# Optimization experiments

Measured on AMD Instinct MI355X. Metric: run time of the kernel, lower is better.

Reference implementation:

```python
import jax, jax.numpy as jnp
import numpy as np

NEG_SLOPE = 0.2  # PyG GATv2Conv default


def with_self_loops(edge_index, n):
    loop = jnp.arange(n, dtype=edge_index.dtype)
    src = jnp.concatenate([edge_index[0], loop])
    dst = jnp.concatenate([edge_index[1], loop])
    return src, dst


def gatv2(x, src, dst, Wl, bl, Wr, br, att, bias):
    """PyG GATv2Conv (eval mode, concat=True, add_self_loops done by caller).
    x: [N, F_in]; att: [H, C]. Returns [N, H*C]."""
    N = x.shape[0]
    H, C = att.shape
    xl = (x @ Wl + bl).reshape(N, H, C)  # lin_l(x): source-side transform
    xr = (x @ Wr + br).reshape(N, H, C)  # lin_r(x): target-side transform
    s = jax.nn.leaky_relu(xl[src] + xr[dst], NEG_SLOPE)      # [E,H,C]
    logit = jnp.einsum('ehc,hc->eh', s, att)                 # [E,H]
    m = jax.ops.segment_max(logit, dst, num_segments=N)      # stable softmax per target
    e = jnp.exp(logit - m[dst])
    den = jax.ops.segment_sum(e, dst, num_segments=N)
    alpha = e / (den[dst] + 1e-16)                           # [E,H]
    out = jax.ops.segment_sum(alpha[:, :, None] * xl[src], dst, num_segments=N)
    return out.reshape(N, H * C) + bias


def setup_inputs() -> dict:
    N, E = 20000, 320000        # agent nodes / edges
    M, EM = 40000, 400000       # lane nodes / edges
    B, L = 64, 50               # focal agents, centerline length
    SEQ, INC, HID, HEADS, OUT = 50, 2, 32, 4, 60
    H4 = HID * HEADS
    key = jax.random.key(0)
    ks = list(jax.random.split(key, 48))
    kit = iter(ks)

    def p(shape):
        return jax.random.normal(next(kit), shape, jnp.float32) * 0.05

    inp = {
        'x': jax.random.normal(next(kit), (N, SEQ, INC), jnp.float32),
        'edge_index': jax.random.randint(next(kit), (2, E), 0, N),
        'lane_x': jax.random.normal(next(kit), (M, 2), jnp.float32),
        'lane_edge_index': jax.random.randint(next(kit), (2, EM), 0, M),
        'batch': jnp.sort(jax.random.randint(next(kit), (N,), 0, B)),
        'focal_idx': jax.random.randint(next(kit), (B,), 0, N),
        'centerlines': jax.random.normal(next(kit), (B, L, 2), jnp.float32),
        # agent embedding
        'ae_W': p((SEQ * INC, HID)), 'ae_b': p((HID,)),
        # agent subgraph conv1 / conv2
        'a1_Wl': p((HID, H4)), 'a1_bl': p((H4,)), 'a1_Wr': p((HID, H4)), 'a1_br': p((H4,)), 'a1_att': p((HEADS, HID)), 'a1_b': p((H4,)),
        'a2_Wl': p((H4, H4)), 'a2_bl': p((H4,)), 'a2_Wr': p((H4, H4)), 'a2_br': p((H4,)), 'a2_att': p((HEADS, HID)), 'a2_b': p((H4,)),
        # map embedding + map subgraph
        'me_W': p((2, HID)), 'me_b': p((HID,)),
        'm1_Wl': p((HID, H4)), 'm1_bl': p((H4,)), 'm1_Wr': p((HID, H4)), 'm1_br': p((H4,)), 'm1_att': p((HEADS, HID)), 'm1_b': p((H4,)),
        'm2_Wl': p((H4, H4)), 'm2_bl': p((H4,)), 'm2_Wr': p((H4, H4)), 'm2_br': p((H4,)), 'm2_att': p((HEADS, HID)), 'm2_b': p((H4,)),
        # centerline processor
        'cl_W': p((2, HID)), 'cl_b': p((HID,)),
        # global graph (heads=1)
        'g_Wl': p((H4, HID)), 'g_bl': p((HID,)), 'g_Wr': p((H4, HID)), 'g_br': p((HID,)), 'g_att': p((1, HID)), 'g_b': p((HID,)),
        # output head
        'fc_W': p((2 * HID, OUT)), 'fc_b': p((OUT,)),
    }
    return inp


def reference(x, edge_index, lane_x, lane_edge_index, batch, focal_idx, centerlines,
              ae_W, ae_b,
              a1_Wl, a1_bl, a1_Wr, a1_br, a1_att, a1_b,
              a2_Wl, a2_bl, a2_Wr, a2_br, a2_att, a2_b,
              me_W, me_b,
              m1_Wl, m1_bl, m1_Wr, m1_br, m1_att, m1_b,
              m2_Wl, m2_bl, m2_Wr, m2_br, m2_att, m2_b,
              cl_W, cl_b,
              g_Wl, g_bl, g_Wr, g_br, g_att, g_b,
              fc_W, fc_b):
    N = x.shape[0]
    M = lane_x.shape[0]
    # agent branch
    agent_x = jax.nn.relu(x.reshape(N, -1) @ ae_W + ae_b)
    a_src, a_dst = with_self_loops(edge_index, N)
    h = jax.nn.relu(gatv2(agent_x, a_src, a_dst, a1_Wl, a1_bl, a1_Wr, a1_br, a1_att, a1_b))
    agent_features = jax.nn.relu(gatv2(h, a_src, a_dst, a2_Wl, a2_bl, a2_Wr, a2_br, a2_att, a2_b))  # [N,128]
    # map branch (output unused downstream in original, computed for faithfulness)
    map_x = jax.nn.relu(lane_x @ me_W + me_b)
    m_src, m_dst = with_self_loops(lane_edge_index, M)
    hm = jax.nn.relu(gatv2(map_x, m_src, m_dst, m1_Wl, m1_bl, m1_Wr, m1_br, m1_att, m1_b))
    map_features = jax.nn.relu(gatv2(hm, m_src, m_dst, m2_Wl, m2_bl, m2_Wr, m2_br, m2_att, m2_b))
    _ = map_features  # global_mean_pool results are dead code in the original forward
    # global graph over agent features (heads=1)
    global_features = jax.nn.relu(gatv2(agent_features, a_src, a_dst, g_Wl, g_bl, g_Wr, g_br, g_att, g_b))  # [N,32]
    focal = global_features[focal_idx]  # [B,32]
    # centerlines: per-polyline mean then linear (no relu, as in original)
    cl_feat = jnp.mean(centerlines, axis=1) @ cl_W + cl_b  # [B,32]
    combined = jnp.concatenate([focal, cl_feat], axis=1)
    return combined @ fc_W + fc_b
```

## Files before the change

### kernel.cpp

```cpp
#include <hip/hip_runtime.h>
#include <hip/hip_bf16.h>
#include <hip/hip_fp16.h>
#include <math.h>

typedef __hip_bfloat16 bf16;
#define NEG_SLOPE 0.2f
#define SFLAG (1 << 30)

typedef _Float16 f16x8 __attribute__((ext_vector_type(8)));
typedef float f32x4 __attribute__((ext_vector_type(4)));

__global__ void k_detect_zero(const unsigned short* __restrict__ x, int* __restrict__ flag,
                              int* __restrict__ zbase, int n) {
    for (int i = blockIdx.x * blockDim.x + threadIdx.x; i < n; i += gridDim.x * blockDim.x)
        zbase[i] = 0;
    if (blockIdx.x == 0) {
        __shared__ int cnt;
        if (threadIdx.x == 0) cnt = 0;
        __syncthreads();
        int local = 0;
        for (int i = threadIdx.x; i < 2048; i += blockDim.x) {
            unsigned short w = x[2 * i];
            int e = (w >> 7) & 0xFF;
            if (e >= 0x90) local++;
        }
        atomicAdd(&cnt, local);
        __syncthreads();
        if (threadIdx.x == 0) flag[0] = (cnt > 100) ? 1 : 0;
    }
}

#define NSEG 25
struct Seg { const void* src; int n; int off; };
struct Tab { Seg s[NSEG]; };

__device__ __forceinline__ float ldconv(const void* src, int i, int f32mode) {
    return f32mode ? ((const float*)src)[i]
                   : __bfloat162float(((const bf16*)src)[i]);
}

__global__ void k_convert(Tab tab, float* __restrict__ dst, const int* __restrict__ flag,
                          const int* __restrict__ dstArr, int E, int N,
                          int* __restrict__ deg, int* __restrict__ rank,
                          const void* a2WlS, const void* a2WrS,
                          const void* gWlS, const void* gWrS,
                          __half* __restrict__ a2Wlt, __half* __restrict__ a2Wrt,
                          __half* __restrict__ gWlt, __half* __restrict__ gWrt) {
    int f32mode = flag[0];
    int gid = blockIdx.x * blockDim.x + threadIdx.x;
    int gsz = gridDim.x * blockDim.x;
    for (int s = 0; s < NSEG; s++) {
        Seg sg = tab.s[s];
        for (int i = gid; i < sg.n; i += gsz) {
            dst[sg.off + i] = ldconv(sg.src, i, f32mode);
        }
    }
    for (int i = gid; i < 128 * 128; i += gsz) {
        int k = i >> 7, j = i & 127;
        a2Wlt[(size_t)j * 128 + k] = __float2half(ldconv(a2WlS, i, f32mode));
        a2Wrt[(size_t)j * 128 + k] = __float2half(ldconv(a2WrS, i, f32mode));
    }
    for (int i = gid; i < 128 * 32; i += gsz) {
        int k = i >> 5, j = i & 31;
        gWlt[(size_t)j * 128 + k] = __float2half(ldconv(gWlS, i, f32mode));
        gWrt[(size_t)j * 128 + k] = __float2half(ldconv(gWrS, i, f32mode));
    }
    int EA = E + N;
    for (int e = gid; e < EA; e += gsz) {
        int d = (e < E) ? dstArr[e] : (e - E);
        rank[e] = atomicAdd(&deg[d], 1);
    }
}

__launch_bounds__(1024)
__global__ void k_scanf(const int* __restrict__ deg, int* __restrict__ offs,
                        int n, int* __restrict__ st, int nb) {
    __shared__ int ws[16];
    __shared__ int stot, sprev;
    int tile = blockIdx.x;
    int i = tile * 1024 + threadIdx.x;
    int lane = threadIdx.x & 63, wid = threadIdx.x >> 6;
    int v = (i < n) ? deg[i] : 0;
    int x = v;
    #pragma unroll
    for (int o = 1; o < 64; o <<= 1) {
        int y = __shfl_up(x, o);
        if (lane >= o) x += y;
    }
    if (lane == 63) ws[wid] = x;
    __syncthreads();
    if (wid == 0) {
        int w = (lane < 16) ? ws[lane] : 0;
        int s = w;
        #pragma unroll
        for (int o = 1; o < 16; o <<= 1) {
            int y = __shfl_up(s, o);
            if (lane >= o) s += y;
        }
        if (lane < 16) ws[lane] = s - w;
        if (lane == 15) stot = s;
    }
    __syncthreads();
    int local = ws[wid] + x - v;
    if (threadIdx.x == 0) {
        int prev = 0;
        if (tile > 0) {
            int vv;
            while ((((vv = __hip_atomic_load(&st[tile - 1], __ATOMIC_ACQUIRE,
                                             __HIP_MEMORY_SCOPE_AGENT))) & SFLAG) == 0) {}
            prev = vv & ~SFLAG;
        }
        __hip_atomic_store(&st[tile], (prev + stot) | SFLAG, __ATOMIC_RELEASE,
                           __HIP_MEMORY_SCOPE_AGENT);
        sprev = prev;
        if (tile == nb - 1) offs[n] = prev + stot;
    }
    __syncthreads();
    if (i < n) offs[i] = sprev + local;
}

__launch_bounds__(256)
__global__ void k_fill_embedlin(const int* __restrict__ srcArr, const int* __restrict__ dstArr,
                                int E, int N, const int* __restrict__ offs,
                                const int* __restrict__ rank, int* __restrict__ csr,
                                const void* __restrict__ xraw, const int* __restrict__ flag,
                                const float* __restrict__ aeW, const float* __restrict__ aeb,
                                const float* __restrict__ Wl, const float* __restrict__ bl,
                                const float* __restrict__ Wr, const float* __restrict__ br,
                                __half* __restrict__ outl, float* __restrict__ outr,
                                int EB) {
    __shared__ float xs[100 * 36];
    __shared__ float axs[32 * 36];
    if (blockIdx.x >= EB) {
        int e = (blockIdx.x - EB) * 256 + threadIdx.x;
        int EA = E + N;
        if (e >= EA) return;
        int d, s;
        if (e < E) { d = dstArr[e]; s = srcArr[e]; } else { d = s = e - E; }
        csr[offs[d] + rank[e]] = s;
        return;
    }
    constexpr int NTP = 36;
    int t = threadIdx.x, nb = blockIdx.x * 32;
    if (flag[0]) {
        const float4* x4 = (const float4*)xraw;
        for (int idx = t; idx < 32 * 25; idx += 256) {
            int node = idx / 25, k4 = idx % 25;
            float4 v = x4[(size_t)(nb + node) * 25 + k4];
            xs[(k4 * 4 + 0) * NTP + node] = v.x;
            xs[(k4 * 4 + 1) * NTP + node] = v.y;
            xs[(k4 * 4 + 2) * NTP + node] = v.z;
            xs[(k4 * 4 + 3) * NTP + node] = v.w;
        }
    } else {
        const ushort4* xu = (const ushort4*)xraw;
        for (int idx = t; idx < 32 * 25; idx += 256) {
            int node = idx / 25, k4 = idx % 25;
            ushort4 u = xu[(size_t)(nb + node) * 25 + k4];
            xs[(k4 * 4 + 0) * NTP + node] = __uint_as_float((unsigned)u.x << 16);
            xs[(k4 * 4 + 1) * NTP + node] = __uint_as_float((unsigned)u.y << 16);
            xs[(k4 * 4 + 2) * NTP + node] = __uint_as_float((unsigned)u.z << 16);
            xs[(k4 * 4 + 3) * NTP + node] = __uint_as_float((unsigned)u.w << 16);
        }
    }
    __syncthreads();
    {
        int j = t & 31, g0 = t >> 5;
        float a0 = 0.f, a1 = 0.f, a2 = 0.f, a3 = 0.f;
        #pragma unroll 10
        for (int k = 0; k < 100; k++) {
            float w = aeW[k * 32 + j];
            const float4 xv = *(const float4*)&xs[k * NTP + g0 * 4];
            a0 += w * xv.x; a1 += w * xv.y; a2 += w * xv.z; a3 += w * xv.w;
        }
        float bj = aeb[j];
        axs[j * NTP + g0 * 4 + 0] = fmaxf(a0 + bj, 0.f);
        axs[j * NTP + g0 * 4 + 1] = fmaxf(a1 + bj, 0.f);
        axs[j * NTP + g0 * 4 + 2] = fmaxf(a2 + bj, 0.f);
        axs[j * NTP + g0 * 4 + 3] = fmaxf(a3 + bj, 0.f);
    }
    __syncthreads();
    {
        int j = t & 63, g0 = t >> 6;
        float aL0[2][4], aL1[2][4], aR0[2][4], aR1[2][4];
        #pragma unroll
        for (int g = 0; g < 2; g++)
            #pragma unroll
            for (int c = 0; c < 4; c++) { aL0[g][c]=0.f; aL1[g][c]=0.f; aR0[g][c]=0.f; aR1[g][c]=0.f; }
        #pragma unroll 4
        for (int k = 0; k < 32; k++) {
            float wl0 = Wl[k * 128 + j];
            float wl1 = Wl[k * 128 + j + 64];
            float wr0 = Wr[k * 128 + j];
            float wr1 = Wr[k * 128 + j + 64];
            #pragma unroll
            for (int g = 0; g < 2; g++) {
                const float4 xv = *(const float4*)&axs[k * NTP + (g0 + g * 4) * 4];
                aL0[g][0] += wl0 * xv.x; aL0[g][1] += wl0 * xv.y; aL0[g][2] += wl0 * xv.z; aL0[g][3] += wl0 * xv.w;
                aL1[g][0] += wl1 * xv.x; aL1[g][1] += wl1 * xv.y; aL1[g][2] += wl1 * xv.z; aL1[g][3] += wl1 * xv.w;
                aR0[g][0] += wr0 * xv.x; aR0[g][1] += wr0 * xv.y; aR0[g][2] += wr0 * xv.z; aR0[g][3] += wr0 * xv.w;
                aR1[g][0] += wr1 * xv.x; aR1[g][1] += wr1 * xv.y; aR1[g][2] += wr1 * xv.z; aR1[g][3] += wr1 * xv.w;
            }
        }
        float bl0 = bl[j], bl1 = bl[j + 64], br0 = br[j], br1 = br[j + 64];
        #pragma unroll
        for (int g = 0; g < 2; g++) {
            int n0 = nb + (g0 + g * 4) * 4;
            #pragma unroll
            for (int c = 0; c < 4; c++) {
                size_t row = (size_t)(n0 + c) * 128;
                outl[row + j]      = __float2half(aL0[g][c] + bl0);
                outl[row + j + 64] = __float2half(aL1[g][c] + bl1);
                outr[row + j]      = aR0[g][c] + br0;
                outr[row + j + 64] = aR1[g][c] + br1;
            }
        }
    }
}

__device__ __forceinline__ void gat_proc(float4 raw, bool valid,
                                         const float* xrd, const float* av,
                                         float* acc, float& sm) {
    const __half2* h = (const __half2*)&raw;
    float v[8];
    float2 f;
    f = __half22float2(h[0]); v[0] = f.x; v[1] = f.y;
    f = __half22float2(h[1]); v[2] = f.x; v[3] = f.y;
    f = __half22float2(h[2]); v[4] = f.x; v[5] = f.y;
    f = __half22float2(h[3]); v[6] = f.x; v[7] = f.y;
    float p = 0.f;
    #pragma unroll
    for (int c = 0; c < 8; c++) {
        float u = v[c] + xrd[c];
        u = (u > 0.f) ? u : NEG_SLOPE * u;
        p += u * av[c];
    }
    p += __shfl_xor(p, 1);
    p += __shfl_xor(p, 2);
    p += __shfl_xor(p, 4);
    p += __shfl_xor(p, 8);
    float w = __expf(fminf(p, 80.f));
    if (!valid) w = 0.f;
    sm += w;
    #pragma unroll
    for (int c = 0; c < 8; c++) acc[c] += w * v[c];
}

__device__ __forceinline__ void gat16_to_lds(__half* xsh,
                                             const __half* __restrict__ xl,
                                             const float* __restrict__ xr,
                                             const float* __restrict__ att,
                                             const int* __restrict__ offs,
                                             const int* __restrict__ csr,
                                             const float* __restrict__ bias,
                                             int d, int node) {
    int t = threadIdx.x;
    int lane = t & 63;
    int sub = lane & 15;
    int lb = lane & 48;
    float av[8];
    {
        const float4* t4 = (const float4*)(att + sub * 8);
        float4 c = t4[0], e = t4[1];
        av[0]=c.x; av[1]=c.y; av[2]=c.z; av[3]=c.w;
        av[4]=e.x; av[5]=e.y; av[6]=e.z; av[7]=e.w;
    }
    bool ok = d >= 0;
    int i0 = ok ? offs[d] : 0;
    int i1 = ok ? offs[d + 1] : 0;
    int cnt = i1 - i0;

    float xrd[8];
    #pragma unroll
    for (int c = 0; c < 8; c++) xrd[c] = 0.f;
    if (ok) {
        const float4* p4 = (const float4*)(xr + (size_t)d * 128 + sub * 8);
        float4 a = p4[0], b = p4[1];
        xrd[0]=a.x; xrd[1]=a.y; xrd[2]=a.z; xrd[3]=a.w;
        xrd[4]=b.x; xrd[5]=b.y; xrd[6]=b.z; xrd[7]=b.w;
    }
    float acc[8];
    #pragma unroll
    for (int c = 0; c < 8; c++) acc[c] = 0.f;
    float sm = 0.f;

    int myv = (sub < cnt) ? csr[i0 + sub] : 0;
    for (int c0 = 0; c0 < cnt; c0 += 16) {
        int myv_nxt = (c0 + 16 + sub < cnt) ? csr[i0 + c0 + 16 + sub] : 0;
        int rem = min(cnt - c0, 16);
        for (int k = 0; k < rem; k += 4) {
            int s0 = __shfl(myv, lb + k + 0);
            int s1 = __shfl(myv, lb + k + 1);
            int s2 = __shfl(myv, lb + k + 2);
            int s3 = __shfl(myv, lb + k + 3);
            float4 r0 = *(const float4*)(xl + (size_t)s0 * 128 + sub * 8);
            float4 r1 = *(const float4*)(xl + (size_t)s1 * 128 + sub * 8);
            float4 r2 = *(const float4*)(xl + (size_t)s2 * 128 + sub * 8);
            float4 r3 = *(const float4*)(xl + (size_t)s3 * 128 + sub * 8);
            gat_proc(r0, true,        xrd, av, acc, sm);
            gat_proc(r1, k + 1 < rem, xrd, av, acc, sm);
            gat_proc(r2, k + 2 < rem, xrd, av, acc, sm);
            gat_proc(r3, k + 3 < rem, xrd, av, acc, sm);
        }
        myv = myv_nxt;
    }

    int ch = sub * 8;
    if (ok) {
        float inv = 1.f / (sm + 1e-16f);
        #pragma unroll
        for (int c = 0; c < 8; c += 2) {
            __half2 hv;
            hv.x = __float2half(fmaxf(acc[c]     * inv + bias[ch + c],     0.f));
            hv.y = __float2half(fmaxf(acc[c + 1] * inv + bias[ch + c + 1], 0.f));
            *(__half2*)&xsh[node * 136 + ch + c] = hv;
        }
    } else {
        #pragma unroll
        for (int c = 0; c < 8; c += 2)
            *(__half2*)&xsh[node * 136 + ch + c] = __half2{__half(0.f), __half(0.f)};
    }
}

__launch_bounds__(256)
__global__ void k_gatlin(const __half* __restrict__ xl, const float* __restrict__ xr,
                         const float* __restrict__ att,
                         const int* __restrict__ offs, const int* __restrict__ csr,
                         const float* __restrict__ bias,
                         const __half* __restrict__ Wlt, const float* __restrict__ bl,
                         const __half* __restrict__ Wrt, const float* __restrict__ br,
                         __half* __restrict__ outl, float* __restrict__ outr, int N,
                         const int* __restrict__ focal, int B,
                         int* __restrict__ L, int* __restrict__ Lcnt, int GT) {
    if (blockIdx.x >= GT) {
        int t = threadIdx.x;
        if (t < B) {
            int f = focal[t];
            int j0 = offs[f], j1 = offs[f + 1];
            int base = atomicAdd(Lcnt, j1 - j0);
            for (int j = j0; j < j1; j++) L[base + (j - j0)] = csr[j];
        }
        return;
    }
    __shared__ __align__(16) __half xsh[16 * 136];
    int nb = blockIdx.x * 16;
    int t = threadIdx.x;
    int lane = t & 63, wv = t >> 6;
    int quad = lane >> 4, n16 = lane & 15;
    {
        int node = wv * 4 + quad;
        int dd = nb + node;
        gat16_to_lds(xsh, xl, xr, att, offs, csr, bias, (dd < N) ? dd : -1, node);
    }
    __syncthreads();

    f16x8 a[4];
    #pragma unroll
    for (int kt = 0; kt < 4; kt++)
        a[kt] = *(const f16x8*)&xsh[n16 * 136 + kt * 32 + quad * 8];

    int j0 = wv * 32;
    f32x4 aL0 = {0.f,0.f,0.f,0.f}, aL1 = {0.f,0.f,0.f,0.f};
    f32x4 aR0 = {0.f,0.f,0.f,0.f}, aR1 = {0.f,0.f,0.f,0.f};
    #pragma unroll
    for (int kt = 0; kt < 4; kt++) {
        int ko = kt * 32 + quad * 8;
        f16x8 b0 = *(const f16x8*)&Wlt[(size_t)(j0 + n16) * 128 + ko];
        f16x8 b1 = *(const f16x8*)&Wlt[(size_t)(j0 + 16 + n16) * 128 + ko];
        f16x8 b2 = *(const f16x8*)&Wrt[(size_t)(j0 + n16) * 128 + ko];
        f16x8 b3 = *(const f16x8*)&Wrt[(size_t)(j0 + 16 + n16) * 128 + ko];
        aL0 = __builtin_amdgcn_mfma_f32_16x16x32_f16(a[kt], b0, aL0, 0, 0, 0);
        aL1 = __builtin_amdgcn_mfma_f32_16x16x32_f16(a[kt], b1, aL1, 0, 0, 0);
        aR0 = __builtin_amdgcn_mfma_f32_16x16x32_f16(a[kt], b2, aR0, 0, 0, 0);
        aR1 = __builtin_amdgcn_mfma_f32_16x16x32_f16(a[kt], b3, aR1, 0, 0, 0);
    }
    float blj0 = bl[j0 + n16], blj1 = bl[j0 + 16 + n16];
    float brj0 = br[j0 + n16], brj1 = br[j0 + 16 + n16];
    #pragma unroll
    for (int r = 0; r < 4; r++) {
        int node = quad * 4 + r;
        if (nb + node >= N) continue;
        size_t row = (size_t)(nb + node) * 128;
        outl[row + j0 + n16]      = __float2half(aL0[r] + blj0);
        outl[row + j0 + 16 + n16] = __float2half(aL1[r] + blj1);
        outr[row + j0 + n16]      = aR0[r] + brj0;
        outr[row + j0 + 16 + n16] = aR1[r] + brj1;
    }
}

__launch_bounds__(256)
__global__ void k_gatling(const __half* __restrict__ xl, const float* __restrict__ xr,
                          const float* __restrict__ att,
                          const int* __restrict__ offs, const int* __restrict__ csr,
                          const float* __restrict__ bias,
                          const __half* __restrict__ Wlt, const float* __restrict__ bl,
                          const __half* __restrict__ Wrt, const float* __restrict__ br,
                          __half* __restrict__ outl, float* __restrict__ outr,
                          const int* __restrict__ L, const int* __restrict__ Lcnt) {
    __shared__ __align__(16) __half xsh[16 * 136];
    int total = *Lcnt;
    int t = threadIdx.x;
    int lane = t & 63, wv = t >> 6;
    int quad = lane >> 4, n16 = lane & 15;

    for (int tile = blockIdx.x; tile * 16 < total; tile += gridDim.x) {
        if (tile != (int)blockIdx.x) __syncthreads();
        int node = wv * 4 + quad;
        int idx = tile * 16 + node;
        int d = (idx < total) ? L[idx] : -1;
        gat16_to_lds(xsh, xl, xr, att, offs, csr, bias, d, node);
        __syncthreads();

        f16x8 a[4];
        #pragma unroll
        for (int kt = 0; kt < 4; kt++)
            a[kt] = *(const f16x8*)&xsh[n16 * 136 + kt * 32 + quad * 8];

        const __half* Wt = (wv < 2) ? Wlt : Wrt;
        int j0 = (wv & 1) * 16;
        f32x4 accv = {0.f,0.f,0.f,0.f};
        #pragma unroll
        for (int kt = 0; kt < 4; kt++) {
            f16x8 b = *(const f16x8*)&Wt[(size_t)(j0 + n16) * 128 + kt * 32 + quad * 8];
            accv = __builtin_amdgcn_mfma_f32_16x16x32_f16(a[kt], b, accv, 0, 0, 0);
        }
        float bj = ((wv < 2) ? bl : br)[j0 + n16];
        #pragma unroll
        for (int r = 0; r < 4; r++) {
            int nn = quad * 4 + r;
            int gidx = tile * 16 + nn;
            if (gidx >= total) continue;
            int gd = L[gidx];
            size_t row = (size_t)gd * 32;
            if (wv < 2) outl[row + j0 + n16] = __float2half(accv[r] + bj);
            else        outr[row + j0 + n16] = accv[r] + bj;
        }
    }
}

__launch_bounds__(64)
__global__ void k_tailf(const __half* __restrict__ xl, const float* __restrict__ xr,
                        const float* __restrict__ att,
                        const int* __restrict__ offs, const int* __restrict__ csr,
                        const float* __restrict__ gb, const int* __restrict__ focal,
                        const float* __restrict__ clf, const float* __restrict__ clW,
                        const float* __restrict__ clb, const float* __restrict__ fcW,
                        const float* __restrict__ fcb, void* __restrict__ out,
                        const int* __restrict__ flag) {
    __shared__ float comb[64];
    __shared__ float ssb[2];
    int b = blockIdx.x;
    int t = threadIdx.x;
    int d = focal[b];
    int grp = t >> 3, sub = t & 7;
    int i0 = offs[d], i1 = offs[d + 1];

    float xrd[4], av[4], acc[4];
    {
        float4 a = *(const float4*)(xr + (size_t)d * 32 + sub * 4);
        xrd[0]=a.x; xrd[1]=a.y; xrd[2]=a.z; xrd[3]=a.w;
        float4 c = *(const float4*)(att + sub * 4);
        av[0]=c.x; av[1]=c.y; av[2]=c.z; av[3]=c.w;
    }
    #pragma unroll
    for (int c = 0; c < 4; c++) acc[c] = 0.f;
    float sm = 0.f;

    for (int i = i0 + grp; i < i1; i += 8) {
        float2 raw = *(const float2*)(xl + (size_t)csr[i] * 32 + sub * 4);
        const __half2* h = (const __half2*)&raw;
        float v[4];
        float2 f;
        f = __half22float2(h[0]); v[0] = f.x; v[1] = f.y;
        f = __half22float2(h[1]); v[2] = f.x; v[3] = f.y;
        float p = 0.f;
        #pragma unroll
        for (int c = 0; c < 4; c++) {
            float u = v[c] + xrd[c];
            u = (u > 0.f) ? u : NEG_SLOPE * u;
            p += u * av[c];
        }
        p += __shfl_xor(p, 1);
        p += __shfl_xor(p, 2);
        p += __shfl_xor(p, 4);
        float w = __expf(fminf(p, 80.f));
        sm += w;
        #pragma unroll
        for (int c = 0; c < 4; c++) acc[c] += w * v[c];
    }
    sm += __shfl_xor(sm, 8); sm += __shfl_xor(sm, 16); sm += __shfl_xor(sm, 32);
    #pragma unroll
    for (int c = 0; c < 4; c++) {
        acc[c] += __shfl_xor(acc[c], 8);
        acc[c] += __shfl_xor(acc[c], 16);
        acc[c] += __shfl_xor(acc[c], 32);
    }
    if (grp == 0) {
        float inv = 1.f / (sm + 1e-16f);
        #pragma unroll
        for (int c = 0; c < 4; c++)
            comb[sub * 4 + c] = fmaxf(acc[c] * inv + gb[sub * 4 + c], 0.f);
    }
    if (t < 2) {
        float s = 0.f;
        for (int l = 0; l < 50; l++) s += clf[(size_t)b * 100 + l * 2 + t];
        ssb[t] = s / 50.f;
    }
    __syncthreads();
    if (t < 32) comb[32 + t] = ssb[0] * clW[t] + ssb[1] * clW[32 + t] + clb[t];
    __syncthreads();
    if (t < 60) {
        float a2 = fcb[t];
        #pragma unroll 16
        for (int k = 0; k < 64; k++) a2 += comb[k] * fcW[k * 60 + t];
        if (flag[0]) ((float*)out)[b * 60 + t] = a2;
        else ((bf16*)out)[b * 60 + t] = __float2bfloat16(a2);
    }
}

extern "C" void kernel_launch(void* const* d_in, const int* in_sizes, int n_in,
                              void* d_out, int out_size, void* d_ws, size_t ws_size,
                              hipStream_t stream) {
    const int* edge  = (const int*)d_in[1];
    const int* focal = (const int*)d_in[5];

    const int N = in_sizes[0] / 100;
    const int E = in_sizes[1] / 2;
    const int B = in_sizes[5];
    const int EA = E + N;
    const int* srcArr = edge;
    const int* dstArr = edge + E;

    const int idxs[NSEG] = {7,8,9,10,11,12,13,14,15,16,17,18,19,20,
                            35,36,37,38,39,40,41,42,43,44, 6};
    float* base = (float*)d_ws;
    int* flag = (int*)base;
    float* wf = base + 16;
    Tab tab;
    int off[NSEG];
    int o = 0;
    for (int i = 0; i < NSEG; i++) {
        tab.s[i].src = d_in[idxs[i]];
        tab.s[i].n   = in_sizes[idxs[i]];
        tab.s[i].off = o;
        off[i] = o;
        o += in_sizes[idxs[i]];
    }
    const float* aeW  = wf + off[0],  *aeb  = wf + off[1];
    const float* a1Wl = wf + off[2],  *a1bl = wf + off[3];
    const float* a1Wr = wf + off[4],  *a1br = wf + off[5];
    const float* a1att= wf + off[6],  *a1b  = wf + off[7];
    const float* a2bl = wf + off[9];
    const float* a2br = wf + off[11];
    const float* a2att= wf + off[12], *a2b  = wf + off[13];
    const float* clW  = wf + off[14], *clb  = wf + off[15];
    const float* gbl  = wf + off[17];
    const float* gbr  = wf + off[19];
    const float* gatt = wf + off[20], *gb   = wf + off[21];
    const float* fcW  = wf + off[22], *fcb  = wf + off[23];
    const float* clf  = wf + off[24];

    float* p = wf + o + ((4 - (o & 3)) & 3);
    size_t N128 = (size_t)N * 128;
    __half* hxl1 = (__half*)p;      p += (size_t)N * 64;
    float* fB1  = p;                p += N128;
    __half* hxl2 = (__half*)p;      p += (size_t)N * 64;
    float* fB2  = p;                p += N128;
    int* deg    = (int*)p;
    int* st     = deg + N;
    int* offs   = st + 32;
    int* rank   = offs + N + 1;
    int* csr    = rank + EA;
    uintptr_t up = (uintptr_t)(csr + EA);
    up = (up + 15) & ~(uintptr_t)15;
    __half* a2Wlt = (__half*)up;
    __half* a2Wrt = a2Wlt + 16384;
    __half* gWlt  = a2Wrt + 16384;
    __half* gWrt  = gWlt + 4096;
    int* Lbuf = (int*)(gWrt + 4096);
    int* Lcnt = st + 30;

    const int NB = (N + 1023) / 1024;
    const int EB = N / 32;
    const int FBLK = (EA + 255) / 256;
    const int GT = (N + 15) / 16;

    k_detect_zero<<<64, 256, 0, stream>>>((const unsigned short*)d_in[0], flag, deg, N + 32);
    k_convert<<<256, 256, 0, stream>>>(tab, wf, flag, dstArr, E, N, deg, rank,
                                       d_in[15], d_in[17], d_in[37], d_in[39],
                                       a2Wlt, a2Wrt, gWlt, gWrt);
    k_scanf<<<NB, 1024, 0, stream>>>(deg, offs, N, st, NB);
    k_fill_embedlin<<<EB + FBLK, 256, 0, stream>>>(srcArr, dstArr, E, N, offs, rank, csr,
                                                   d_in[0], flag, aeW, aeb,
                                                   a1Wl, a1bl, a1Wr, a1br, hxl1, fB1, EB);
    k_gatlin<<<GT + 1, 256, 0, stream>>>(hxl1, fB1, a1att, offs, csr, a1b,
                                         a2Wlt, a2bl, a2Wrt, a2br, hxl2, fB2, N,
                                         focal, B, Lbuf, Lcnt, GT);
    k_gatling<<<128, 256, 0, stream>>>(hxl2, fB2, a2att, offs, csr, a2b,
                                       gWlt, gbl, gWrt, gbr, hxl1, fB1, Lbuf, Lcnt);
    k_tailf<<<B, 64, 0, stream>>>(hxl1, fB1, gatt, offs, csr, gb, focal,
                                  clf, clW, clb, fcW, fcb, d_out, flag);
}
```

Baseline: 255.7 us.

## Compute layer-2 target transform only for needed nodes; single-block degree scan

After: 256.7 us. Within noise of the previous version (+0.4%).

```diff
diff --git a/kernel.cpp b/kernel.cpp
--- a/kernel.cpp
+++ b/kernel.cpp
@@ -5,7 +5,6 @@
 
 typedef __hip_bfloat16 bf16;
 #define NEG_SLOPE 0.2f
-#define SFLAG (1 << 30)
 
 typedef _Float16 f16x8 __attribute__((ext_vector_type(8)));
 typedef float f32x4 __attribute__((ext_vector_type(4)));
@@ -73,50 +72,47 @@
 }
 
 __launch_bounds__(1024)
-__global__ void k_scanf(const int* __restrict__ deg, int* __restrict__ offs,
-                        int n, int* __restrict__ st, int nb) {
+__global__ void k_scans(const int* __restrict__ deg, int* __restrict__ offs, int n) {
     __shared__ int ws[16];
-    __shared__ int stot, sprev;
-    int tile = blockIdx.x;
-    int i = tile * 1024 + threadIdx.x;
-    int lane = threadIdx.x & 63, wid = threadIdx.x >> 6;
-    int v = (i < n) ? deg[i] : 0;
-    int x = v;
-    #pragma unroll
-    for (int o = 1; o < 64; o <<= 1) {
-        int y = __shfl_up(x, o);
-        if (lane >= o) x += y;
-    }
-    if (lane == 63) ws[wid] = x;
-    __syncthreads();
-    if (wid == 0) {
-        int w = (lane < 16) ? ws[lane] : 0;
-        int s = w;
-        #pragma unroll
-        for (int o = 1; o < 16; o <<= 1) {
-            int y = __shfl_up(s, o);
-            if (lane >= o) s += y;
-        }
-        if (lane < 16) ws[lane] = s - w;
-        if (lane == 15) stot = s;
-    }
-    __syncthreads();
-    int local = ws[wid] + x - v;
-    if (threadIdx.x == 0) {
-        int prev = 0;
-        if (tile > 0) {
-            int vv;
-            while ((((vv = __hip_atomic_load(&st[tile - 1], __ATOMIC_ACQUIRE,
-                                             __HIP_MEMORY_SCOPE_AGENT))) & SFLAG) == 0) {}
-            prev = vv & ~SFLAG;
-        }
-        __hip_atomic_store(&st[tile], (prev + stot) | SFLAG, __ATOMIC_RELEASE,
-                           __HIP_MEMORY_SCOPE_AGENT);
-        sprev = prev;
-        if (tile == nb - 1) offs[n] = prev + stot;
-    }
-    __syncthreads();
-    if (i < n) offs[i] = sprev + local;
+    __shared__ int stot_s;
+    __shared__ int carry_s;
+    int t = threadIdx.x;
+    if (t == 0) carry_s = 0;
+    int lane = t & 63, wid = t >> 6;
+    int nt = (n + 1023) >> 10;
+    int vnext = (t < n) ? deg[t] : 0;
+    for (int tile = 0; tile < nt; tile++) {
+        int i = tile * 1024 + t;
+        int v = vnext;
+        int inx = i + 1024;
+        vnext = (tile + 1 < nt && inx < n) ? deg[inx] : 0;
+        int x = v;
+        #pragma unroll
+        for (int o = 1; o < 64; o <<= 1) {
+            int y = __shfl_up(x, o);
+            if (lane >= o) x += y;
+        }
+        if (lane == 63) ws[wid] = x;
+        __syncthreads();
+        if (wid == 0) {
+            int w = (lane < 16) ? ws[lane] : 0;
+            int s = w;
+            #pragma unroll
+            for (int o = 1; o < 16; o <<= 1) {
+                int y = __shfl_up(s, o);
+                if (lane >= o) s += y;
+            }
+            if (lane < 16) ws[lane] = s - w;
+            if (lane == 15) stot_s = s;
+        }
+        __syncthreads();
+        int cprev = carry_s;
+        if (i < n) offs[i] = cprev + ws[wid] + x - v;
+        __syncthreads();
+        if (t == 0) carry_s = cprev + stot_s;
+        __syncthreads();
+    }
+    if (t == 0) offs[n] = carry_s;
 }
 
 __launch_bounds__(256)
@@ -248,7 +244,7 @@
 
 __device__ __forceinline__ void gat16_to_lds(__half* xsh,
                                              const __half* __restrict__ xl,
-                                             const float* __restrict__ xr,
+                                             const float* xrp,
                                              const float* __restrict__ att,
                                              const int* __restrict__ offs,
                                              const int* __restrict__ csr,
@@ -274,7 +270,7 @@
     #pragma unroll
     for (int c = 0; c < 8; c++) xrd[c] = 0.f;
     if (ok) {
-        const float4* p4 = (const float4*)(xr + (size_t)d * 128 + sub * 8);
+        const float4* p4 = (const float4*)(xrp + sub * 8);
         float4 a = p4[0], b = p4[1];
         xrd[0]=a.x; xrd[1]=a.y; xrd[2]=a.z; xrd[3]=a.w;
         xrd[4]=b.x; xrd[5]=b.y; xrd[6]=b.z; xrd[7]=b.w;
@@ -328,8 +324,7 @@
                          const int* __restrict__ offs, const int* __restrict__ csr,
                          const float* __restrict__ bias,
                          const __half* __restrict__ Wlt, const float* __restrict__ bl,
-                         const __half* __restrict__ Wrt, const float* __restrict__ br,
-                         __half* __restrict__ outl, float* __restrict__ outr, int N,
+                         __half* __restrict__ outl, __half* __restrict__ outf1, int N,
                          const int* __restrict__ focal, int B,
                          int* __restrict__ L, int* __restrict__ Lcnt, int GT) {
     if (blockIdx.x >= GT) {
@@ -350,9 +345,18 @@
     {
         int node = wv * 4 + quad;
         int dd = nb + node;
-        gat16_to_lds(xsh, xl, xr, att, offs, csr, bias, (dd < N) ? dd : -1, node);
+        bool okd = dd < N;
+        const float* xrp = xr + (size_t)(okd ? dd : 0) * 128;
+        gat16_to_lds(xsh, xl, xrp, att, offs, csr, bias, okd ? dd : -1, node);
     }
     __syncthreads();
+
+    {
+        int node = t >> 4, ch = (t & 15) * 8;
+        if (nb + node < N)
+            *(f16x8*)&outf1[(size_t)(nb + node) * 128 + ch] =
+                *(const f16x8*)&xsh[node * 136 + ch];
+    }
 
     f16x8 a[4];
     #pragma unroll
@@ -361,21 +365,15 @@
 
     int j0 = wv * 32;
     f32x4 aL0 = {0.f,0.f,0.f,0.f}, aL1 = {0.f,0.f,0.f,0.f};
-    f32x4 aR0 = {0.f,0.f,0.f,0.f}, aR1 = {0.f,0.f,0.f,0.f};
     #pragma unroll
     for (int kt = 0; kt < 4; kt++) {
         int ko = kt * 32 + quad * 8;
         f16x8 b0 = *(const f16x8*)&Wlt[(size_t)(j0 + n16) * 128 + ko];
         f16x8 b1 = *(const f16x8*)&Wlt[(size_t)(j0 + 16 + n16) * 128 + ko];
-        f16x8 b2 = *(const f16x8*)&Wrt[(size_t)(j0 + n16) * 128 + ko];
-        f16x8 b3 = *(const f16x8*)&Wrt[(size_t)(j0 + 16 + n16) * 128 + ko];
         aL0 = __builtin_amdgcn_mfma_f32_16x16x32_f16(a[kt], b0, aL0, 0, 0, 0);
         aL1 = __builtin_amdgcn_mfma_f32_16x16x32_f16(a[kt], b1, aL1, 0, 0, 0);
-        aR0 = __builtin_amdgcn_mfma_f32_16x16x32_f16(a[kt], b2, aR0, 0, 0, 0);
-        aR1 = __builtin_amdgcn_mfma_f32_16x16x32_f16(a[kt], b3, aR1, 0, 0, 0);
     }
     float blj0 = bl[j0 + n16], blj1 = bl[j0 + 16 + n16];
-    float brj0 = br[j0 + n16], brj1 = br[j0 + 16 + n16];
     #pragma unroll
     for (int r = 0; r < 4; r++) {
         int node = quad * 4 + r;
@@ -383,13 +381,14 @@
         size_t row = (size_t)(nb + node) * 128;
         outl[row + j0 + n16]      = __float2half(aL0[r] + blj0);
         outl[row + j0 + 16 + n16] = __float2half(aL1[r] + blj1);
-        outr[row + j0 + n16]      = aR0[r] + brj0;
-        outr[row + j0 + 16 + n16] = aR1[r] + brj1;
     }
 }
 
 __launch_bounds__(256)
-__global__ void k_gatling(const __half* __restrict__ xl, const float* __restrict__ xr,
+__global__ void k_gatling(const __half* __restrict__ xl,
+                          const __half* __restrict__ hf1,
+                          const __half* __restrict__ Wrt2,
+                          const float* __restrict__ br2,
                           const float* __restrict__ att,
                           const int* __restrict__ offs, const int* __restrict__ csr,
                           const float* __restrict__ bias,
@@ -398,6 +397,7 @@
                           __half* __restrict__ outl, float* __restrict__ outr,
                           const int* __restrict__ L, const int* __restrict__ Lcnt) {
     __shared__ __align__(16) __half xsh[16 * 136];
+    __shared__ __align__(16) float xr2[16 * 132];
     int total = *Lcnt;
     int t = threadIdx.x;
     int lane = t & 63, wv = t >> 6;
@@ -405,12 +405,44 @@
 
     for (int tile = blockIdx.x; tile * 16 < total; tile += gridDim.x) {
         if (tile != (int)blockIdx.x) __syncthreads();
+        {
+            int ia = tile * 16 + n16;
+            int da = (ia < total) ? L[ia] : -1;
+            f16x8 af[4];
+            if (da >= 0) {
+                #pragma unroll
+                for (int kt = 0; kt < 4; kt++)
+                    af[kt] = *(const f16x8*)&hf1[(size_t)da * 128 + kt * 32 + quad * 8];
+            } else {
+                #pragma unroll
+                for (int kt = 0; kt < 4; kt++)
+                    #pragma unroll
+                    for (int c = 0; c < 8; c++) af[kt][c] = (_Float16)0;
+            }
+            f32x4 ar0 = {0.f,0.f,0.f,0.f}, ar1 = {0.f,0.f,0.f,0.f};
+            #pragma unroll
+            for (int kt = 0; kt < 4; kt++) {
+                int ko = kt * 32 + quad * 8;
+                f16x8 b0 = *(const f16x8*)&Wrt2[(size_t)(wv * 32 + n16) * 128 + ko];
+                f16x8 b1 = *(const f16x8*)&Wrt2[(size_t)(wv * 32 + 16 + n16) * 128 + ko];
+                ar0 = __builtin_amdgcn_mfma_f32_16x16x32_f16(af[kt], b0, ar0, 0, 0, 0);
+                ar1 = __builtin_amdgcn_mfma_f32_16x16x32_f16(af[kt], b1, ar1, 0, 0, 0);
+            }
+            int c0 = wv * 32 + n16, c1 = wv * 32 + 16 + n16;
+            float bb0 = br2[c0], bb1 = br2[c1];
+            #pragma unroll
+            for (int r = 0; r < 4; r++) {
+                int row = quad * 4 + r;
+                xr2[row * 132 + c0] = ar0[r] + bb0;
+                xr2[row * 132 + c1] = ar1[r] + bb1;
+            }
+        }
+        __syncthreads();
         int node = wv * 4 + quad;
         int idx = tile * 16 + node;
         int d = (idx < total) ? L[idx] : -1;
-        gat16_to_lds(xsh, xl, xr, att, offs, csr, bias, d, node);
-        __syncthreads();
-
+        gat16_to_lds(xsh, xl, &xr2[node * 132], att, offs, csr, bias, d, node);
+        __syncthreads();
         f16x8 a[4];
         #pragma unroll
         for (int kt = 0; kt < 4; kt++)
@@ -565,7 +597,7 @@
     __half* hxl1 = (__half*)p;      p += (size_t)N * 64;
     float* fB1  = p;                p += N128;
     __half* hxl2 = (__half*)p;      p += (size_t)N * 64;
-    float* fB2  = p;                p += N128;
+    __half* hf1  = (__half*)p;      p += (size_t)N * 64;
     int* deg    = (int*)p;
     int* st     = deg + N;
     int* offs   = st + 32;
@@ -580,7 +612,6 @@
     int* Lbuf = (int*)(gWrt + 4096);
     int* Lcnt = st + 30;
 
-    const int NB = (N + 1023) / 1024;
     const int EB = N / 32;
     const int FBLK = (EA + 255) / 256;
     const int GT = (N + 15) / 16;
@@ -589,14 +620,14 @@
     k_convert<<<256, 256, 0, stream>>>(tab, wf, flag, dstArr, E, N, deg, rank,
                                        d_in[15], d_in[17], d_in[37], d_in[39],
                                        a2Wlt, a2Wrt, gWlt, gWrt);
-    k_scanf<<<NB, 1024, 0, stream>>>(deg, offs, N, st, NB);
+    k_scans<<<1, 1024, 0, stream>>>(deg, offs, N);
     k_fill_embedlin<<<EB + FBLK, 256, 0, stream>>>(srcArr, dstArr, E, N, offs, rank, csr,
                                                    d_in[0], flag, aeW, aeb,
                                                    a1Wl, a1bl, a1Wr, a1br, hxl1, fB1, EB);
     k_gatlin<<<GT + 1, 256, 0, stream>>>(hxl1, fB1, a1att, offs, csr, a1b,
-                                         a2Wlt, a2bl, a2Wrt, a2br, hxl2, fB2, N,
+                                         a2Wlt, a2bl, hxl2, hf1, N,
                                          focal, B, Lbuf, Lcnt, GT);
-    k_gatling<<<128, 256, 0, stream>>>(hxl2, fB2, a2att, offs, csr, a2b,
+    k_gatling<<<128, 256, 0, stream>>>(hxl2, hf1, a2Wrt, a2br, a2att, offs, csr, a2b,
                                        gWlt, gbl, gWrt, gbr, hxl1, fB1, Lbuf, Lcnt);
     k_tailf<<<B, 64, 0, stream>>>(hxl1, fB1, gatt, offs, csr, gb, focal,
                                   clf, clW, clb, fcW, fcb, d_out, flag);
```
